# Kernel optimization log

Measured on AMD Instinct MI355X. Metric: run time of the kernel, lower is better.

Reference implementation:

```python
import jax, jax.numpy as jnp
import numpy as np

B, N, D = 8, 192, 768   # batch of docs, events per doc, embed_dim
H = 150                 # Score hidden_dim
PAD = -1000.0           # pad_and_stack fill value


def setup_inputs() -> dict:
    key = jax.random.key(0)
    ks = jax.random.split(key, 7)
    s1 = 1.0 / np.sqrt(3 * D)
    s2 = 1.0 / np.sqrt(H)
    return {
        "event_embed": jax.random.normal(ks[0], (B, N, D), jnp.float32),
        "W1": jax.random.normal(ks[1], (3 * D, H), jnp.float32) * s1,
        "b1": jnp.zeros((H,), jnp.float32),
        "W2": jax.random.normal(ks[2], (H, H), jnp.float32) * s2,
        "b2": jnp.zeros((H,), jnp.float32),
        "W3": jax.random.normal(ks[3], (H, 1), jnp.float32) * s2,
        "b3": jnp.zeros((1,), jnp.float32),
    }


def reference(event_embed, W1, b1, W2, b2, W3, b3):
    Bq, Nq, Dq = event_embed.shape
    # antecedent pairs: for each event i, all k < i (row-major, matches torch loop order)
    rows, cols = jnp.tril_indices(Nq, k=-1)          # [P], P = N*(N-1)/2
    i_g = event_embed[:, rows]                        # [B, P, D]
    j_g = event_embed[:, cols]                        # [B, P, D]
    pairs = jnp.concatenate([i_g, j_g, i_g * j_g], axis=-1)  # [B, P, 3D]
    # Score MLP (dropout is identity at inference)
    h = jax.nn.relu(pairs @ W1 + b1)                  # [B, P, H]
    h = jax.nn.relu(h @ W2 + b2)                      # [B, P, H]
    s = (h @ W3 + b3)[..., 0]                         # [B, P]
    # Scatter pair scores into [B, N, N]; diagonal stays 0 = epsilon score.
    logits = jnp.zeros((Bq, Nq, Nq), event_embed.dtype).at[:, rows, cols].set(s)
    tri = jnp.tril(jnp.ones((Nq, Nq), dtype=bool))    # valid cols: k <= i (incl epsilon)
    masked = jnp.where(tri, logits, -jnp.inf)
    probs = jax.nn.softmax(masked, axis=-1)           # ragged softmax per event row
    return jnp.where(tri, probs, jnp.asarray(PAD, probs.dtype))  # pad_and_stack(value=-1000)
```

## Files before the change

### kernel.cpp

```cpp
#include <hip/hip_runtime.h>
#include <hip/hip_bf16.h>

#define NSEQ   192
#define PADV   -1000.0f
#define NEGINF -1.0e30f

typedef __bf16 bf16x8 __attribute__((ext_vector_type(8)));
typedef float  f32x4  __attribute__((ext_vector_type(4)));

__device__ __forceinline__ void glds16(const void* g, void* l) {
  __builtin_amdgcn_global_load_lds(
      (const __attribute__((address_space(1))) unsigned int*)g,
      (__attribute__((address_space(3))) unsigned int*)l, 16, 0, 0);
}

#define MFMA16(a, b, c) __builtin_amdgcn_mfma_f32_16x16x32_bf16((a), (b), (c), 0, 0, 0)

__global__ __launch_bounds__(256) void prep_pack(const float* __restrict__ W1,
                                                 const float* __restrict__ W2,
                                                 const float* __restrict__ b1,
                                                 __bf16* __restrict__ W1abp,
                                                 __bf16* __restrict__ W1cp,
                                                 __bf16* __restrict__ W2p,
                                                 float* __restrict__ b1p,
                                                 float* __restrict__ A12) {
  int idx = blockIdx.x * 256 + threadIdx.x;
  if (idx < 394240) A12[idx] = 0.f;
  if (idx < 97280)  A12[394240 + idx] = 0.f;

  if (idx < 245760) {
    int e = idx & 7, l = (idx >> 3) & 63, t = idx >> 9;
    int ct = t % 20, kk = t / 20;
    int k = kk * 32 + ((l >> 4) << 3) + e;
    int hp = ct * 16 + (l & 15);
    int col = (hp < 160) ? hp : hp - 160;
    int rbase = (hp < 160) ? 0 : 768;
    float v = (col < 150) ? W1[(size_t)(rbase + k) * 150 + col] : 0.f;
    W1abp[idx] = (__bf16)v;
  } else if (idx < 368640) {
    int j = idx - 245760;
    int e = j & 7, l = (j >> 3) & 63, t = j >> 9;
    int ct = t % 10, kk = t / 10;
    int k = kk * 32 + ((l >> 4) << 3) + e;
    int h = ct * 16 + (l & 15);
    float v = (h < 150) ? W1[(size_t)(1536 + k) * 150 + h] : 0.f;
    W1cp[j] = (__bf16)v;
  } else if (idx < 394240) {
    int j = idx - 368640;
    int e = j & 7, l = (j >> 3) & 63, t = j >> 9;
    int ct = t % 10, s = t / 10;
    int k = s * 32 + ((l >> 4) << 3) + e;
    int h = ct * 16 + (l & 15);
    float v = (k < 150 && h < 150) ? W2[(size_t)k * 150 + h] : 0.f;
    W2p[j] = (__bf16)v;
  } else if (idx < 394400) {
    int h = idx - 394240;
    b1p[h] = (h < 150) ? b1[h] : 0.f;
  }
}

__global__ __launch_bounds__(256) void prep_gemm(const float* __restrict__ E,
                                                 const __bf16* __restrict__ W1abp,
                                                 float* __restrict__ A12) {
  int tid = threadIdx.x;
  int w = tid >> 6, l = tid & 63, m = l & 15, kg = l >> 4;
  int mt = blockIdx.x >> 3;
  int c  = blockIdx.x & 7;
  const float* ep = E + (size_t)(mt * 16 + m) * 768 + c * 96;

  f32x4 acc[5];
#pragma unroll
  for (int u = 0; u < 5; ++u) acc[u] = (f32x4){0.f, 0.f, 0.f, 0.f};

#pragma unroll
  for (int kk = 0; kk < 3; ++kk) {
    int k = kk * 32 + kg * 8;
    f32x4 x0 = *(const f32x4*)(ep + k);
    f32x4 x1 = *(const f32x4*)(ep + k + 4);
    bf16x8 af;
#pragma unroll
    for (int e = 0; e < 4; ++e) { af[e] = (__bf16)x0[e]; af[e + 4] = (__bf16)x1[e]; }
    const bf16x8* wp = (const bf16x8*)W1abp + (size_t)(((c * 3 + kk) * 20) + w * 5) * 64 + l;
#pragma unroll
    for (int u = 0; u < 5; ++u)
      acc[u] = MFMA16(af, wp[u * 64], acc[u]);
  }
#pragma unroll
  for (int u = 0; u < 5; ++u)
#pragma unroll
    for (int r = 0; r < 4; ++r)
      atomicAdd(&A12[(size_t)(mt * 16 + kg * 4 + r) * 320 + (w * 5 + u) * 16 + m], acc[u][r]);
}

__global__ __launch_bounds__(256) void pair_mlp(
    const float* __restrict__ E, const float* __restrict__ A12,
    const __bf16* __restrict__ W1cp, const __bf16* __restrict__ W2p,
    const float* __restrict__ b1p, const float* __restrict__ b2,
    const float* __restrict__ W3, const float* __restrict__ b3,
    float* __restrict__ out) {
  __shared__ alignas(16) char pool[149504];
  char* eib = pool + 40960;
  char* ejb = pool + 65536;

  const int tid = threadIdx.x;
  const int w = tid >> 6, l = tid & 63;
  const int m = l & 15, kg = l >> 4;

  int bid = blockIdx.x;
  int blk = (bid & 7) * 78 + (bid >> 3);
  int b = blk / 78, r0 = blk - b * 78;
  int it = (int)((sqrtf(8.f * (float)r0 + 1.f) - 1.f) * 0.5f);
  while (it * (it + 1) / 2 > r0) --it;
  while ((it + 1) * (it + 2) / 2 <= r0) ++it;
  int jt = r0 - it * (it + 1) / 2;

  const int ibase = b * NSEQ + it * 16;
  const int jbase = b * NSEQ + jt * 16;

#pragma unroll
  for (int q = 0; q < 5; ++q)
    glds16(W1cp + (size_t)(w * 5 + q) * 512 + l * 8, pool + (w * 5 + q) * 1024);

#pragma unroll
  for (int q = 0; q < 12; ++q) {
    int t = tid + 256 * q;
    int isI = (t < 1536);
    int tt = isI ? t : t - 1536;
    int r = tt / 96, d = tt - (tt / 96) * 96;
    int sc = d ^ (r & 7);
    const float* src = E + (size_t)((isI ? ibase : jbase) + r) * 768 + sc * 8;
    f32x4 a0 = *(const f32x4*)(src);
    f32x4 a1 = *(const f32x4*)(src + 4);
    bf16x8 v;
#pragma unroll
    for (int e = 0; e < 4; ++e) { v[e] = (__bf16)a0[e]; v[e + 4] = (__bf16)a1[e]; }
    *(bf16x8*)((isI ? eib : ejb) + r * 1536 + d * 16) = v;
  }

  if (tid < 160) {
    float* bwf = (float*)(pool + 90112);
    bwf[tid]       = (tid < 150) ? b2[tid] : 0.f;
    bwf[160 + tid] = (tid < 150) ? W3[tid] : 0.f;
  }
  float b3v = b3[0];

  f32x4 acc1[10][4];
#pragma unroll
  for (int ct = 0; ct < 10; ++ct) {
    f32x4 a1v = *(const f32x4*)(A12 + (size_t)(ibase + m) * 320 + ct * 16 + kg * 4);
    f32x4 b1v = *(const f32x4*)(b1p + ct * 16 + kg * 4);
#pragma unroll
    for (int pt = 0; pt < 4; ++pt) {
      f32x4 a2v = *(const f32x4*)(A12 + (size_t)(jbase + w * 4 + pt) * 320 + 160 + ct * 16 + kg * 4);
      acc1[ct][pt] = a1v + a2v + b1v;
    }
  }

  __syncthreads();

  auto compute = [&](int t) {
    const __bf16* wb = (const __bf16*)(pool + (t & 1) * 20480);
#pragma unroll
    for (int s = 0; s < 2; ++s) {
      int cb = t * 8 + s * 4 + kg;
      bf16x8 eiv = *(const bf16x8*)(eib + m * 1536 + ((cb ^ (m & 7)) << 4));
      float eif[8];
#pragma unroll
      for (int e = 0; e < 8; ++e) eif[e] = (float)eiv[e];
      bf16x8 pf[4];
#pragma unroll
      for (int pt = 0; pt < 4; ++pt) {
        int jr = w * 4 + pt;
        bf16x8 ejv = *(const bf16x8*)(ejb + jr * 1536 + ((cb ^ (jr & 7)) << 4));
#pragma unroll
        for (int e = 0; e < 8; ++e)
          pf[pt][e] = (__bf16)(eif[e] * (float)ejv[e]);
      }
#pragma unroll
      for (int ct = 0; ct < 10; ++ct) {
        bf16x8 wf = *(const bf16x8*)(wb + (s * 10 + ct) * 512 + l * 8);
#pragma unroll
        for (int pt = 0; pt < 4; ++pt)
          acc1[ct][pt] = MFMA16(wf, pf[pt], acc1[ct][pt]);
      }
    }
  };

  for (int t = 0; t < 12; ++t) {
    if (t < 11) {
#pragma unroll
      for (int q = 0; q < 5; ++q)
        glds16(W1cp + ((size_t)(t + 1) * 20 + w * 5 + q) * 512 + l * 8,
               pool + ((t + 1) & 1) * 20480 + (w * 5 + q) * 1024);
      asm volatile("s_waitcnt vmcnt(5)" ::: "memory");
    } else {
      asm volatile("s_waitcnt vmcnt(0)" ::: "memory");
    }
    __builtin_amdgcn_s_barrier();
    compute(t);
    __builtin_amdgcn_s_barrier();
  }

  {
    int f0 = (w < 2) ? w * 13 : 26 + (w - 2) * 12;
    int nf = (w < 2) ? 13 : 12;
    for (int q = 0; q < nf; ++q)
      glds16(W2p + (size_t)(f0 + q) * 512 + l * 8, pool + (f0 + q) * 1024);
  }
#pragma unroll
  for (int pt = 0; pt < 4; ++pt) {
    char* hbp = pool + 51200 + (w * 4 + pt) * 6144;
#pragma unroll
    for (int ct = 0; ct < 10; ++ct) {
      union { __bf16 h[4]; unsigned u[2]; } cv;
      cv.h[0] = (__bf16)fmaxf(acc1[ct][pt][0], 0.f);
      cv.h[1] = (__bf16)fmaxf(acc1[ct][pt][1], 0.f);
      cv.h[2] = (__bf16)fmaxf(acc1[ct][pt][2], 0.f);
      cv.h[3] = (__bf16)fmaxf(acc1[ct][pt][3], 0.f);
      int c = (2 * ct + (kg >> 1)) ^ (m & 7);
      char* dst = hbp + m * 384 + c * 16 + (kg & 1) * 8;
      *(unsigned*)(dst)     = cv.u[0];
      *(unsigned*)(dst + 4) = cv.u[1];
    }
  }
  asm volatile("s_waitcnt vmcnt(0)" ::: "memory");
  __builtin_amdgcn_s_barrier();

  f32x4 acc2[10][4];
#pragma unroll
  for (int ct = 0; ct < 10; ++ct)
#pragma unroll
    for (int pt = 0; pt < 4; ++pt) acc2[ct][pt] = (f32x4){0.f, 0.f, 0.f, 0.f};

#pragma unroll
  for (int s = 0; s < 5; ++s) {
    bf16x8 hf[4];
#pragma unroll
    for (int pt = 0; pt < 4; ++pt)
      hf[pt] = *(const bf16x8*)(pool + 51200 + (w * 4 + pt) * 6144 + m * 384 +
                                (((4 * s + kg) ^ (m & 7)) << 4));
#pragma unroll
    for (int ct = 0; ct < 10; ++ct) {
      bf16x8 w2f = *(const bf16x8*)(pool + (s * 10 + ct) * 1024 + l * 16);
#pragma unroll
      for (int pt = 0; pt < 4; ++pt)
        acc2[ct][pt] = MFMA16(w2f, hf[pt], acc2[ct][pt]);
    }
  }

  const float* bwp = (const float*)(pool + 90112);
#pragma unroll
  for (int pt = 0; pt < 4; ++pt) {
    float sum = 0.f;
#pragma unroll
    for (int ct = 0; ct < 10; ++ct) {
      f32x4 b2q = *(const f32x4*)(bwp + ct * 16 + kg * 4);
      f32x4 w3q = *(const f32x4*)(bwp + 160 + ct * 16 + kg * 4);
#pragma unroll
      for (int r2 = 0; r2 < 4; ++r2)
        sum += fmaxf(acc2[ct][pt][r2] + b2q[r2], 0.f) * w3q[r2];
    }
    sum += __shfl_xor(sum, 16, 64);
    sum += __shfl_xor(sum, 32, 64);
    if (kg == 0) {
      int il = it * 16 + m;
      int jl = jt * 16 + w * 4 + pt;
      if (jl < il)
        out[(size_t)(b * NSEQ + il) * NSEQ + jl] = sum + b3v;
    }
  }
}

__global__ __launch_bounds__(256) void softmax_rows(float* __restrict__ out) {
  int w = threadIdx.x >> 6, l = threadIdx.x & 63;
  int blk = blockIdx.x * 4 + w;
  int i = blk % NSEQ;
  size_t base = (size_t)blk * NSEQ;
  float v[3];
  float mx = NEGINF;
#pragma unroll
  for (int t = 0; t < 3; ++t) {
    int j = l + 64 * t;
    float x = (j < i) ? out[base + j] : (j == i ? 0.f : NEGINF);
    v[t] = x;
    mx = fmaxf(mx, x);
  }
#pragma unroll
  for (int off = 32; off >= 1; off >>= 1) mx = fmaxf(mx, __shfl_xor(mx, off, 64));
  float s = 0.f;
#pragma unroll
  for (int t = 0; t < 3; ++t) s += __expf(v[t] - mx);
#pragma unroll
  for (int off = 32; off >= 1; off >>= 1) s += __shfl_xor(s, off, 64);
  float inv = 1.0f / s;
#pragma unroll
  for (int t = 0; t < 3; ++t) {
    int j = l + 64 * t;
    out[base + j] = (j <= i) ? __expf(v[t] - mx) * inv : PADV;
  }
}

extern "C" void kernel_launch(void* const* d_in, const int* in_sizes, int n_in,
                              void* d_out, int out_size, void* d_ws, size_t ws_size,
                              hipStream_t stream) {
  const float* E  = (const float*)d_in[0];
  const float* W1 = (const float*)d_in[1];
  const float* b1 = (const float*)d_in[2];
  const float* W2 = (const float*)d_in[3];
  const float* b2 = (const float*)d_in[4];
  const float* W3 = (const float*)d_in[5];
  const float* b3 = (const float*)d_in[6];
  float* out = (float*)d_out;

  char* ws = (char*)d_ws;
  float*  A12   = (float*)(ws);
  __bf16* W1abp = (__bf16*)(ws + 1966080);
  __bf16* W1cp  = (__bf16*)(ws + 2457600);
  __bf16* W2p   = (__bf16*)(ws + 2703360);
  float*  b1p   = (float*)(ws + 2754560);

  prep_pack<<<1541, 256, 0, stream>>>(W1, W2, b1, W1abp, W1cp, W2p, b1p, A12);
  prep_gemm<<<768, 256, 0, stream>>>(E, W1abp, A12);
  pair_mlp<<<624, 256, 0, stream>>>(E, A12, W1cp, W2p, b1p, b2, W3, b3, out);
  softmax_rows<<<384, 256, 0, stream>>>(out);
}
```

Baseline: 106.1 us.

## Shrink pair_mlp LDS for two blocks per CU and switch to fp16 MFMA

Switches all packed operands and MFMAs from bf16 to fp16. The i*j product is now a packed fp16 vector multiply instead of a float round-trip. The pair_mlp shared-memory pool drops from ~146KB to ~73KB by staging W1c and W2 in smaller double-buffered chunks (24 and 10 stages). The layer-2 GEMM is split into two passes over half the pair columns, so h1 reuses the E buffers and acc2 registers are halved. With launch_bounds(256,2) this targets two resident blocks per CU to hide latency, at the cost of more barriers and fp16 range/precision risk.

```diff
diff --git a/kernel.cpp b/kernel.cpp
--- a/kernel.cpp
+++ b/kernel.cpp
@@ -5,8 +5,8 @@
 #define PADV   -1000.0f
 #define NEGINF -1.0e30f
 
-typedef __bf16 bf16x8 __attribute__((ext_vector_type(8)));
-typedef float  f32x4  __attribute__((ext_vector_type(4)));
+typedef _Float16 f16x8 __attribute__((ext_vector_type(8)));
+typedef float    f32x4 __attribute__((ext_vector_type(4)));
 
 __device__ __forceinline__ void glds16(const void* g, void* l) {
   __builtin_amdgcn_global_load_lds(
@@ -14,19 +14,18 @@
       (__attribute__((address_space(3))) unsigned int*)l, 16, 0, 0);
 }
 
-#define MFMA16(a, b, c) __builtin_amdgcn_mfma_f32_16x16x32_bf16((a), (b), (c), 0, 0, 0)
+#define MFMA16(a, b, c) __builtin_amdgcn_mfma_f32_16x16x32_f16((a), (b), (c), 0, 0, 0)
 
 __global__ __launch_bounds__(256) void prep_pack(const float* __restrict__ W1,
                                                  const float* __restrict__ W2,
                                                  const float* __restrict__ b1,
-                                                 __bf16* __restrict__ W1abp,
-                                                 __bf16* __restrict__ W1cp,
-                                                 __bf16* __restrict__ W2p,
+                                                 _Float16* __restrict__ W1abp,
+                                                 _Float16* __restrict__ W1cp,
+                                                 _Float16* __restrict__ W2p,
                                                  float* __restrict__ b1p,
                                                  float* __restrict__ A12) {
   int idx = blockIdx.x * 256 + threadIdx.x;
-  if (idx < 394240) A12[idx] = 0.f;
-  if (idx < 97280)  A12[394240 + idx] = 0.f;
+  if (idx < 245760) { A12[idx] = 0.f; A12[245760 + idx] = 0.f; }
 
   if (idx < 245760) {
     int e = idx & 7, l = (idx >> 3) & 63, t = idx >> 9;
@@ -36,31 +35,31 @@
     int col = (hp < 160) ? hp : hp - 160;
     int rbase = (hp < 160) ? 0 : 768;
     float v = (col < 150) ? W1[(size_t)(rbase + k) * 150 + col] : 0.f;
-    W1abp[idx] = (__bf16)v;
-  } else if (idx < 368640) {
+    W1abp[idx] = (_Float16)v;
+  } else if (idx < 393216) {
     int j = idx - 245760;
-    int e = j & 7, l = (j >> 3) & 63, t = j >> 9;
-    int ct = t % 10, kk = t / 10;
+    int kk = j / 6144, rem = j % 6144;
+    int q = rem >> 9, l = (rem >> 3) & 63, e = rem & 7;
     int k = kk * 32 + ((l >> 4) << 3) + e;
-    int h = ct * 16 + (l & 15);
-    float v = (h < 150) ? W1[(size_t)(1536 + k) * 150 + h] : 0.f;
-    W1cp[j] = (__bf16)v;
-  } else if (idx < 394240) {
-    int j = idx - 368640;
-    int e = j & 7, l = (j >> 3) & 63, t = j >> 9;
-    int ct = t % 10, s = t / 10;
+    int h = q * 16 + (l & 15);
+    float v = (q < 10 && h < 150) ? W1[(size_t)(1536 + k) * 150 + h] : 0.f;
+    W1cp[j] = (_Float16)v;
+  } else if (idx < 423936) {
+    int j = idx - 393216;
+    int s = j / 6144, rem = j % 6144;
+    int q = rem >> 9, l = (rem >> 3) & 63, e = rem & 7;
     int k = s * 32 + ((l >> 4) << 3) + e;
-    int h = ct * 16 + (l & 15);
-    float v = (k < 150 && h < 150) ? W2[(size_t)k * 150 + h] : 0.f;
-    W2p[j] = (__bf16)v;
-  } else if (idx < 394400) {
-    int h = idx - 394240;
+    int h = q * 16 + (l & 15);
+    float v = (q < 10 && k < 150 && h < 150) ? W2[(size_t)k * 150 + h] : 0.f;
+    W2p[j] = (_Float16)v;
+  } else if (idx < 424096) {
+    int h = idx - 423936;
     b1p[h] = (h < 150) ? b1[h] : 0.f;
   }
 }
 
 __global__ __launch_bounds__(256) void prep_gemm(const float* __restrict__ E,
-                                                 const __bf16* __restrict__ W1abp,
+                                                 const _Float16* __restrict__ W1abp,
                                                  float* __restrict__ A12) {
   int tid = threadIdx.x;
   int w = tid >> 6, l = tid & 63, m = l & 15, kg = l >> 4;
@@ -77,10 +76,10 @@
     int k = kk * 32 + kg * 8;
     f32x4 x0 = *(const f32x4*)(ep + k);
     f32x4 x1 = *(const f32x4*)(ep + k + 4);
-    bf16x8 af;
-#pragma unroll
-    for (int e = 0; e < 4; ++e) { af[e] = (__bf16)x0[e]; af[e + 4] = (__bf16)x1[e]; }
-    const bf16x8* wp = (const bf16x8*)W1abp + (size_t)(((c * 3 + kk) * 20) + w * 5) * 64 + l;
+    f16x8 af;
+#pragma unroll
+    for (int e = 0; e < 4; ++e) { af[e] = (_Float16)x0[e]; af[e + 4] = (_Float16)x1[e]; }
+    const f16x8* wp = (const f16x8*)W1abp + (size_t)(((c * 3 + kk) * 20) + w * 5) * 64 + l;
 #pragma unroll
     for (int u = 0; u < 5; ++u)
       acc[u] = MFMA16(af, wp[u * 64], acc[u]);
@@ -92,15 +91,15 @@
       atomicAdd(&A12[(size_t)(mt * 16 + kg * 4 + r) * 320 + (w * 5 + u) * 16 + m], acc[u][r]);
 }
 
-__global__ __launch_bounds__(256) void pair_mlp(
+__global__ __launch_bounds__(256, 2) void pair_mlp(
     const float* __restrict__ E, const float* __restrict__ A12,
-    const __bf16* __restrict__ W1cp, const __bf16* __restrict__ W2p,
+    const _Float16* __restrict__ W1cp, const _Float16* __restrict__ W2p,
     const float* __restrict__ b1p, const float* __restrict__ b2,
     const float* __restrict__ W3, const float* __restrict__ b3,
     float* __restrict__ out) {
-  __shared__ alignas(16) char pool[149504];
-  char* eib = pool + 40960;
-  char* ejb = pool + 65536;
+  __shared__ alignas(16) char pool[75008];
+  char* eib = pool + 24576;
+  char* ejb = pool + 49152;
 
   const int tid = threadIdx.x;
   const int w = tid >> 6, l = tid & 63;
@@ -118,8 +117,8 @@
   const int jbase = b * NSEQ + jt * 16;
 
 #pragma unroll
-  for (int q = 0; q < 5; ++q)
-    glds16(W1cp + (size_t)(w * 5 + q) * 512 + l * 8, pool + (w * 5 + q) * 1024);
+  for (int q = 0; q < 3; ++q)
+    glds16(W1cp + (size_t)(w * 3 + q) * 512 + l * 8, pool + (w * 3 + q) * 1024);
 
 #pragma unroll
   for (int q = 0; q < 12; ++q) {
@@ -131,14 +130,14 @@
     const float* src = E + (size_t)((isI ? ibase : jbase) + r) * 768 + sc * 8;
     f32x4 a0 = *(const f32x4*)(src);
     f32x4 a1 = *(const f32x4*)(src + 4);
-    bf16x8 v;
-#pragma unroll
-    for (int e = 0; e < 4; ++e) { v[e] = (__bf16)a0[e]; v[e + 4] = (__bf16)a1[e]; }
-    *(bf16x8*)((isI ? eib : ejb) + r * 1536 + d * 16) = v;
+    f16x8 v;
+#pragma unroll
+    for (int e = 0; e < 4; ++e) { v[e] = (_Float16)a0[e]; v[e + 4] = (_Float16)a1[e]; }
+    *(f16x8*)((isI ? eib : ejb) + r * 1536 + d * 16) = v;
   }
 
   if (tid < 160) {
-    float* bwf = (float*)(pool + 90112);
+    float* bwf = (float*)(pool + 73728);
     bwf[tid]       = (tid < 150) ? b2[tid] : 0.f;
     bwf[160 + tid] = (tid < 150) ? W3[tid] : 0.f;
   }
@@ -158,116 +157,131 @@
 
   __syncthreads();
 
-  auto compute = [&](int t) {
-    const __bf16* wb = (const __bf16*)(pool + (t & 1) * 20480);
-#pragma unroll
-    for (int s = 0; s < 2; ++s) {
-      int cb = t * 8 + s * 4 + kg;
-      bf16x8 eiv = *(const bf16x8*)(eib + m * 1536 + ((cb ^ (m & 7)) << 4));
-      float eif[8];
-#pragma unroll
-      for (int e = 0; e < 8; ++e) eif[e] = (float)eiv[e];
-      bf16x8 pf[4];
-#pragma unroll
-      for (int pt = 0; pt < 4; ++pt) {
-        int jr = w * 4 + pt;
-        bf16x8 ejv = *(const bf16x8*)(ejb + jr * 1536 + ((cb ^ (jr & 7)) << 4));
-#pragma unroll
-        for (int e = 0; e < 8; ++e)
-          pf[pt][e] = (__bf16)(eif[e] * (float)ejv[e]);
-      }
-#pragma unroll
-      for (int ct = 0; ct < 10; ++ct) {
-        bf16x8 wf = *(const bf16x8*)(wb + (s * 10 + ct) * 512 + l * 8);
-#pragma unroll
-        for (int pt = 0; pt < 4; ++pt)
-          acc1[ct][pt] = MFMA16(wf, pf[pt], acc1[ct][pt]);
-      }
-    }
-  };
-
-  for (int t = 0; t < 12; ++t) {
-    if (t < 11) {
-#pragma unroll
-      for (int q = 0; q < 5; ++q)
-        glds16(W1cp + ((size_t)(t + 1) * 20 + w * 5 + q) * 512 + l * 8,
-               pool + ((t + 1) & 1) * 20480 + (w * 5 + q) * 1024);
-      asm volatile("s_waitcnt vmcnt(5)" ::: "memory");
+  for (int t = 0; t < 24; ++t) {
+    if (t < 23) {
+#pragma unroll
+      for (int q = 0; q < 3; ++q)
+        glds16(W1cp + ((size_t)(t + 1) * 12 + w * 3 + q) * 512 + l * 8,
+               pool + ((t + 1) & 1) * 12288 + (w * 3 + q) * 1024);
+      asm volatile("s_waitcnt vmcnt(3)" ::: "memory");
     } else {
       asm volatile("s_waitcnt vmcnt(0)" ::: "memory");
     }
     __builtin_amdgcn_s_barrier();
-    compute(t);
+
+    const char* wb = pool + (t & 1) * 12288;
+    int cb = t * 4 + kg;
+    f16x8 eiv = *(const f16x8*)(eib + m * 1536 + ((cb ^ (m & 7)) << 4));
+    f16x8 pf[4];
+#pragma unroll
+    for (int pt = 0; pt < 4; ++pt) {
+      int jr = w * 4 + pt;
+      f16x8 ejv = *(const f16x8*)(ejb + jr * 1536 + ((cb ^ (jr & 7)) << 4));
+      pf[pt] = eiv * ejv;
+    }
+#pragma unroll
+    for (int ct = 0; ct < 10; ++ct) {
+      f16x8 wf = *(const f16x8*)(wb + ct * 1024 + l * 16);
+#pragma unroll
+      for (int pt = 0; pt < 4; ++pt)
+        acc1[ct][pt] = MFMA16(wf, pf[pt], acc1[ct][pt]);
+    }
     __builtin_amdgcn_s_barrier();
   }
 
-  {
-    int f0 = (w < 2) ? w * 13 : 26 + (w - 2) * 12;
-    int nf = (w < 2) ? 13 : 12;
-    for (int q = 0; q < nf; ++q)
-      glds16(W2p + (size_t)(f0 + q) * 512 + l * 8, pool + (f0 + q) * 1024);
-  }
-#pragma unroll
-  for (int pt = 0; pt < 4; ++pt) {
-    char* hbp = pool + 51200 + (w * 4 + pt) * 6144;
+  auto write_h1 = [&](int c, int pt) {
+    char* hbp = eib + (w * 2 + c) * 6144;
 #pragma unroll
     for (int ct = 0; ct < 10; ++ct) {
-      union { __bf16 h[4]; unsigned u[2]; } cv;
-      cv.h[0] = (__bf16)fmaxf(acc1[ct][pt][0], 0.f);
-      cv.h[1] = (__bf16)fmaxf(acc1[ct][pt][1], 0.f);
-      cv.h[2] = (__bf16)fmaxf(acc1[ct][pt][2], 0.f);
-      cv.h[3] = (__bf16)fmaxf(acc1[ct][pt][3], 0.f);
-      int c = (2 * ct + (kg >> 1)) ^ (m & 7);
-      char* dst = hbp + m * 384 + c * 16 + (kg & 1) * 8;
+      union { _Float16 h[4]; unsigned u[2]; } cv;
+      cv.h[0] = (_Float16)fmaxf(acc1[ct][pt][0], 0.f);
+      cv.h[1] = (_Float16)fmaxf(acc1[ct][pt][1], 0.f);
+      cv.h[2] = (_Float16)fmaxf(acc1[ct][pt][2], 0.f);
+      cv.h[3] = (_Float16)fmaxf(acc1[ct][pt][3], 0.f);
+      int cc = (2 * ct + (kg >> 1)) ^ (m & 7);
+      char* dst = hbp + m * 384 + cc * 16 + (kg & 1) * 8;
       *(unsigned*)(dst)     = cv.u[0];
       *(unsigned*)(dst + 4) = cv.u[1];
     }
-  }
-  asm volatile("s_waitcnt vmcnt(0)" ::: "memory");
-  __builtin_amdgcn_s_barrier();
-
-  f32x4 acc2[10][4];
-#pragma unroll
-  for (int ct = 0; ct < 10; ++ct)
-#pragma unroll
-    for (int pt = 0; pt < 4; ++pt) acc2[ct][pt] = (f32x4){0.f, 0.f, 0.f, 0.f};
-
-#pragma unroll
-  for (int s = 0; s < 5; ++s) {
-    bf16x8 hf[4];
-#pragma unroll
-    for (int pt = 0; pt < 4; ++pt)
-      hf[pt] = *(const bf16x8*)(pool + 51200 + (w * 4 + pt) * 6144 + m * 384 +
-                                (((4 * s + kg) ^ (m & 7)) << 4));
+  };
+
+#pragma unroll
+  for (int q = 0; q < 3; ++q)
+    glds16(W2p + (size_t)(w * 3 + q) * 512 + l * 8, pool + (w * 3 + q) * 1024);
+  write_h1(0, 0);
+  write_h1(1, 1);
+
+  f32x4 acc2[10][2];
+  float sums[2][2];
+
+#pragma unroll
+  for (int r = 0; r < 10; ++r) {
+    const int p = r / 5, s = r - p * 5;
+    if (r < 9) {
+      int ns = (r + 1 >= 5) ? r + 1 - 5 : r + 1;
+#pragma unroll
+      for (int q = 0; q < 3; ++q)
+        glds16(W2p + ((size_t)ns * 12 + w * 3 + q) * 512 + l * 8,
+               pool + ((r + 1) & 1) * 12288 + (w * 3 + q) * 1024);
+      asm volatile("s_waitcnt vmcnt(3)" ::: "memory");
+    } else {
+      asm volatile("s_waitcnt vmcnt(0)" ::: "memory");
+    }
+    __builtin_amdgcn_s_barrier();
+
+    if (r == 5) { write_h1(0, 2); write_h1(1, 3); }
+    if (s == 0) {
+#pragma unroll
+      for (int ct = 0; ct < 10; ++ct) {
+        acc2[ct][0] = (f32x4){0.f, 0.f, 0.f, 0.f};
+        acc2[ct][1] = (f32x4){0.f, 0.f, 0.f, 0.f};
+      }
+    }
+
+    const char* wb = pool + (r & 1) * 12288;
+    f16x8 hf[2];
+#pragma unroll
+    for (int c = 0; c < 2; ++c)
+      hf[c] = *(const f16x8*)(eib + (w * 2 + c) * 6144 + m * 384 +
+                              (((4 * s + kg) ^ (m & 7)) << 4));
 #pragma unroll
     for (int ct = 0; ct < 10; ++ct) {
-      bf16x8 w2f = *(const bf16x8*)(pool + (s * 10 + ct) * 1024 + l * 16);
-#pragma unroll
-      for (int pt = 0; pt < 4; ++pt)
-        acc2[ct][pt] = MFMA16(w2f, hf[pt], acc2[ct][pt]);
-    }
-  }
-
-  const float* bwp = (const float*)(pool + 90112);
-#pragma unroll
-  for (int pt = 0; pt < 4; ++pt) {
-    float sum = 0.f;
-#pragma unroll
-    for (int ct = 0; ct < 10; ++ct) {
-      f32x4 b2q = *(const f32x4*)(bwp + ct * 16 + kg * 4);
-      f32x4 w3q = *(const f32x4*)(bwp + 160 + ct * 16 + kg * 4);
-#pragma unroll
-      for (int r2 = 0; r2 < 4; ++r2)
-        sum += fmaxf(acc2[ct][pt][r2] + b2q[r2], 0.f) * w3q[r2];
-    }
-    sum += __shfl_xor(sum, 16, 64);
-    sum += __shfl_xor(sum, 32, 64);
-    if (kg == 0) {
-      int il = it * 16 + m;
-      int jl = jt * 16 + w * 4 + pt;
-      if (jl < il)
-        out[(size_t)(b * NSEQ + il) * NSEQ + jl] = sum + b3v;
-    }
+      f16x8 wf = *(const f16x8*)(wb + ct * 1024 + l * 16);
+      acc2[ct][0] = MFMA16(wf, hf[0], acc2[ct][0]);
+      acc2[ct][1] = MFMA16(wf, hf[1], acc2[ct][1]);
+    }
+
+    if (s == 4) {
+      const float* bwp = (const float*)(pool + 73728);
+#pragma unroll
+      for (int c = 0; c < 2; ++c) {
+        float sum = 0.f;
+#pragma unroll
+        for (int ct = 0; ct < 10; ++ct) {
+          f32x4 b2q = *(const f32x4*)(bwp + ct * 16 + kg * 4);
+          f32x4 w3q = *(const f32x4*)(bwp + 160 + ct * 16 + kg * 4);
+#pragma unroll
+          for (int r2 = 0; r2 < 4; ++r2)
+            sum += fmaxf(acc2[ct][c][r2] + b2q[r2], 0.f) * w3q[r2];
+        }
+        sum += __shfl_xor(sum, 16, 64);
+        sum += __shfl_xor(sum, 32, 64);
+        sums[p][c] = sum;
+      }
+    }
+    __builtin_amdgcn_s_barrier();
+  }
+
+  if (kg == 0) {
+    int il = it * 16 + m;
+#pragma unroll
+    for (int p = 0; p < 2; ++p)
+#pragma unroll
+      for (int c = 0; c < 2; ++c) {
+        int jl = jt * 16 + w * 4 + p * 2 + c;
+        if (jl < il)
+          out[(size_t)(b * NSEQ + il) * NSEQ + jl] = sums[p][c] + b3v;
+      }
   }
 }
 
@@ -313,13 +327,13 @@
   float* out = (float*)d_out;
 
   char* ws = (char*)d_ws;
-  float*  A12   = (float*)(ws);
-  __bf16* W1abp = (__bf16*)(ws + 1966080);
-  __bf16* W1cp  = (__bf16*)(ws + 2457600);
-  __bf16* W2p   = (__bf16*)(ws + 2703360);
-  float*  b1p   = (float*)(ws + 2754560);
-
-  prep_pack<<<1541, 256, 0, stream>>>(W1, W2, b1, W1abp, W1cp, W2p, b1p, A12);
+  float*    A12   = (float*)(ws);
+  _Float16* W1abp = (_Float16*)(ws + 1966080);
+  _Float16* W1cp  = (_Float16*)(ws + 2457600);
+  _Float16* W2p   = (_Float16*)(ws + 2752512);
+  float*    b1p   = (float*)(ws + 2813952);
+
+  prep_pack<<<1657, 256, 0, stream>>>(W1, W2, b1, W1abp, W1cp, W2p, b1p, A12);
   prep_gemm<<<768, 256, 0, stream>>>(E, W1abp, A12);
   pair_mlp<<<624, 256, 0, stream>>>(E, A12, W1cp, W2p, b1p, b2, W3, b3, out);
   softmax_rows<<<384, 256, 0, stream>>>(out);
```

New measurement: 93.95 us. 11.5% less time.
